# Kernel tuning notes

Measured on AMD Instinct MI355X. Metric: run time of the kernel, lower is better.

The kernel has to match this reference:

```python
import jax, jax.numpy as jnp
import numpy as np

B, N = 16, 200000
R = 1_000_000
ITERS = 5
DAMPING = 0.5


def setup_inputs() -> dict:
    key = jax.random.key(0)
    ks = jax.random.split(key, 7)
    return {
        "evidence_logits": jax.random.normal(ks[0], (B, N), dtype=jnp.float32),
        "weights_t1": jax.random.uniform(ks[1], (R,), dtype=jnp.float32),
        "weights_t2": jax.random.uniform(ks[2], (R,), dtype=jnp.float32),
        "weights_t3": jax.random.uniform(ks[3], (R,), dtype=jnp.float32),
        "indices_t1": jax.random.randint(ks[4], (R, 2), 0, N, dtype=jnp.int64) if jax.config.jax_enable_x64 else jax.random.randint(ks[4], (R, 2), 0, N, dtype=jnp.int32),
        "indices_t2": jax.random.randint(ks[5], (R, 3), 0, N, dtype=jnp.int32),
        "indices_t3": jax.random.randint(ks[6], (R, 3), 0, N, dtype=jnp.int32),
    }


def _t1_messages(q, idx, w):
    # Template T1: p_a -> p_c
    a, c = idx[:, 0], idx[:, 1]
    q_a = q[:, a]            # (B, R)
    q_c = q[:, c]
    wb = w[None, :]
    delta = jnp.zeros_like(q)
    delta = delta.at[:, c].add(wb * q_a)
    delta = delta.at[:, a].add(wb * (q_c - 1.0))
    return delta


def _t2_messages(q, idx, w):
    # Template T2: p_a ^ p_b -> p_c
    a, b, c = idx[:, 0], idx[:, 1], idx[:, 2]
    q_a, q_b, q_c = q[:, a], q[:, b], q[:, c]
    wb = w[None, :]
    delta = jnp.zeros_like(q)
    delta = delta.at[:, c].add(wb * q_a * q_b)
    delta = delta.at[:, a].add(wb * q_b * (q_c - 1.0))
    delta = delta.at[:, b].add(wb * q_a * (q_c - 1.0))
    return delta


def _t3_messages(q, idx, w):
    # Template T3: p_a ^ !p_b -> p_c
    a, b, c = idx[:, 0], idx[:, 1], idx[:, 2]
    q_a, q_b, q_c = q[:, a], q[:, b], q[:, c]
    wb = w[None, :]
    delta = jnp.zeros_like(q)
    delta = delta.at[:, c].add(wb * q_a * (1.0 - q_b))
    delta = delta.at[:, a].add(wb * (1.0 - q_b) * (q_c - 1.0))
    delta = delta.at[:, b].add(wb * q_a * (1.0 - q_c))
    return delta


def reference(evidence_logits, weights_t1, weights_t2, weights_t3,
              indices_t1, indices_t2, indices_t3):
    curr_logits = evidence_logits
    curr_q = jax.nn.sigmoid(curr_logits)
    for _ in range(ITERS):
        total = (_t1_messages(curr_q, indices_t1, weights_t1)
                 + _t2_messages(curr_q, indices_t2, weights_t2)
                 + _t3_messages(curr_q, indices_t3, weights_t3))
        target_logits = evidence_logits + total
        curr_logits = (1.0 - DAMPING) * curr_logits + DAMPING * target_logits
        curr_q = jax.nn.sigmoid(curr_logits)
    return curr_q
```

## Files before the change

### kernel.cpp

```cpp
#include <hip/hip_runtime.h>

#define B 16
#define NN 200000
#define R 1000000
#define ITERS 5
#define E_TOT (8 * R)
#define SCAN_B 1024

typedef unsigned int uint;

__device__ __forceinline__ float sigmoidf_(float x) {
    return 1.0f / (1.0f + __expf(-x));
}


__global__ void cavi_zero_u32(uint* __restrict__ p, int n) {
    int i = blockIdx.x * blockDim.x + threadIdx.x;
    if (i < n) p[i] = 0u;
}

__global__ void cavi_count(const int* __restrict__ i1, const int* __restrict__ i2,
                           const int* __restrict__ i3, uint* __restrict__ cnt) {
    int e = blockIdx.x * blockDim.x + threadIdx.x;
    if (e >= R) return;
    int a1 = i1[2 * e], c1 = i1[2 * e + 1];
    atomicAdd(&cnt[c1], 1u); atomicAdd(&cnt[a1], 1u);
    int a2 = i2[3 * e], b2 = i2[3 * e + 1], c2 = i2[3 * e + 2];
    atomicAdd(&cnt[c2], 1u); atomicAdd(&cnt[a2], 1u); atomicAdd(&cnt[b2], 1u);
    int a3 = i3[3 * e], b3 = i3[3 * e + 1], c3 = i3[3 * e + 2];
    atomicAdd(&cnt[c3], 1u); atomicAdd(&cnt[a3], 1u); atomicAdd(&cnt[b3], 1u);
}

__global__ void cavi_scan1(uint* __restrict__ cnt, uint* __restrict__ bsum) {
    __shared__ uint s[SCAN_B];
    int i = blockIdx.x * SCAN_B + threadIdx.x;
    uint v = (i < NN) ? cnt[i] : 0u;
    s[threadIdx.x] = v;
    __syncthreads();
    for (int d = 1; d < SCAN_B; d <<= 1) {
        uint t = (threadIdx.x >= d) ? s[threadIdx.x - d] : 0u;
        __syncthreads();
        s[threadIdx.x] += t;
        __syncthreads();
    }
    if (i < NN) cnt[i] = s[threadIdx.x] - v;
    if (threadIdx.x == SCAN_B - 1) bsum[blockIdx.x] = s[threadIdx.x];
}

__global__ void cavi_scan2(uint* __restrict__ bsum, int nb) {
    __shared__ uint s[256];
    uint v = (threadIdx.x < (uint)nb) ? bsum[threadIdx.x] : 0u;
    s[threadIdx.x] = v;
    __syncthreads();
    for (int d = 1; d < 256; d <<= 1) {
        uint t = (threadIdx.x >= d) ? s[threadIdx.x - d] : 0u;
        __syncthreads();
        s[threadIdx.x] += t;
        __syncthreads();
    }
    if (threadIdx.x < (uint)nb) bsum[threadIdx.x] = s[threadIdx.x] - v;
    if (threadIdx.x == 255) bsum[nb] = s[255];
}

__global__ void cavi_scan3(const uint* __restrict__ cnt, const uint* __restrict__ bsum,
                           uint* __restrict__ off, uint* __restrict__ cursor, int nb) {
    int i = blockIdx.x * blockDim.x + threadIdx.x;
    if (i < NN) {
        uint v = cnt[i] + bsum[i >> 10];
        off[i] = v;
        cursor[i] = v;
    } else if (i == NN) {
        off[NN] = bsum[nb];
    }
}

__device__ __forceinline__ void put_entry(int dest, int s1, uint md1, int s2, uint md2, float w,
                                          uint* __restrict__ cursor, uint* __restrict__ m0,
                                          uint* __restrict__ m1, float* __restrict__ wf) {
    uint pos = atomicAdd(&cursor[dest], 1u);
    m0[pos] = (uint)s1 | (md1 << 18);
    m1[pos] = (uint)s2 | (md2 << 18);
    wf[pos] = w;
}

__global__ void cavi_fill(const int* __restrict__ i1, const float* __restrict__ w1,
                          const int* __restrict__ i2, const float* __restrict__ w2,
                          const int* __restrict__ i3, const float* __restrict__ w3,
                          uint* __restrict__ cursor, uint* __restrict__ m0,
                          uint* __restrict__ m1, float* __restrict__ wf) {
    int e = blockIdx.x * blockDim.x + threadIdx.x;
    if (e >= R) return;
    {
        int a = i1[2 * e], c = i1[2 * e + 1];
        float w = w1[e];
        put_entry(c, a, 0u, 0, 3u, w, cursor, m0, m1, wf);
        put_entry(a, c, 1u, 0, 3u, w, cursor, m0, m1, wf);
    }
    {
        int a = i2[3 * e], b = i2[3 * e + 1], c = i2[3 * e + 2];
        float w = w2[e];
        put_entry(c, a, 0u, b, 0u, w, cursor, m0, m1, wf);
        put_entry(a, b, 0u, c, 1u, w, cursor, m0, m1, wf);
        put_entry(b, a, 0u, c, 1u, w, cursor, m0, m1, wf);
    }
    {
        int a = i3[3 * e], b = i3[3 * e + 1], c = i3[3 * e + 2];
        float w = w3[e];
        put_entry(c, a, 0u, b, 2u, w, cursor, m0, m1, wf);
        put_entry(a, b, 2u, c, 1u, w, cursor, m0, m1, wf);
        put_entry(b, a, 0u, c, 2u, w, cursor, m0, m1, wf);
    }
}


__global__ void cavi_init_tp(const float* __restrict__ ev, float* __restrict__ ev_nb,
                             float* __restrict__ logits_nb, float* __restrict__ q0) {
    __shared__ float lds[64 * 17];
    int n0 = blockIdx.x * 64;
    #pragma unroll
    for (int p = 0; p < 4; ++p) {
        int idx = p * 256 + threadIdx.x;
        int b = idx >> 6, i = idx & 63;
        lds[i * 17 + b] = ev[b * NN + n0 + i];
    }
    __syncthreads();
    #pragma unroll
    for (int p = 0; p < 4; ++p) {
        int j = p * 256 + threadIdx.x;
        int i = j >> 4, b = j & 15;
        float v = lds[i * 17 + b];
        int o = n0 * B + j;
        ev_nb[o] = v;
        logits_nb[o] = v;
        q0[o] = sigmoidf_(v);
    }
}

__global__ void cavi_out_tp(const float* __restrict__ q_nb, float* __restrict__ out) {
    __shared__ float lds[64 * 17];
    int n0 = blockIdx.x * 64;
    #pragma unroll
    for (int p = 0; p < 4; ++p) {
        int j = p * 256 + threadIdx.x;
        int i = j >> 4, b = j & 15;
        lds[i * 17 + b] = q_nb[n0 * B + j];
    }
    __syncthreads();
    #pragma unroll
    for (int p = 0; p < 4; ++p) {
        int idx = p * 256 + threadIdx.x;
        int b = idx >> 6, i = idx & 63;
        out[b * NN + n0 + i] = lds[i * 17 + b];
    }
}


__global__ void cavi_main(const uint* __restrict__ off,
                          const uint* __restrict__ m0, const uint* __restrict__ m1,
                          const float* __restrict__ wf,
                          const float* __restrict__ ev_nb, float* __restrict__ logits_nb,
                          const float* __restrict__ q_in, float* __restrict__ q_out) {
    int t = blockIdx.x * blockDim.x + threadIdx.x;
    if (t >= NN * B) return;
    int n = t >> 4, b = t & 15;
    uint k0 = off[n], k1 = off[n + 1];
    float acc = 0.0f;
    for (uint k = k0; k < k1; ++k) {
        uint a0 = m0[k], a1 = m1[k];
        float w = wf[k];
        float x = q_in[((a0 & 0x3FFFFu) << 4) + b];
        uint md1 = a0 >> 18;
        x = (md1 == 0u) ? x : ((md1 == 1u) ? x - 1.0f : 1.0f - x);
        uint md2 = a1 >> 18;
        float y = 1.0f;
        if (md2 != 3u) {
            float q2 = q_in[((a1 & 0x3FFFFu) << 4) + b];
            y = (md2 == 0u) ? q2 : ((md2 == 1u) ? q2 - 1.0f : 1.0f - q2);
        }
        acc = fmaf(w * x, y, acc);
    }
    float nl = 0.5f * logits_nb[t] + 0.5f * (ev_nb[t] + acc);
    logits_nb[t] = nl;
    q_out[t] = sigmoidf_(nl);
}


__global__ void fb_init(const float* __restrict__ ev, float* __restrict__ logits,
                        float* __restrict__ q_nb, float* __restrict__ delta_nb) {
    int i = blockIdx.x * blockDim.x + threadIdx.x;
    if (i >= NN * B) return;
    int b = i & 15, n = i >> 4;
    float e = ev[b * NN + n];
    logits[b * NN + n] = e;
    q_nb[i] = sigmoidf_(e);
    delta_nb[i] = 0.0f;
}

__global__ void fb_edges(const float* __restrict__ q, float* __restrict__ delta,
                         const int* __restrict__ idx1, const float* __restrict__ w1,
                         const int* __restrict__ idx2, const float* __restrict__ w2,
                         const int* __restrict__ idx3, const float* __restrict__ w3) {
    int gid = blockIdx.x * blockDim.x + threadIdx.x;
    int b = gid & 15;
    int e = gid >> 4;
    if (e >= 3 * R) return;
    if (e < R) {
        int a = idx1[e * 2 + 0], c = idx1[e * 2 + 1];
        float w = w1[e];
        float qa = q[a * B + b], qc = q[c * B + b];
        atomicAdd(&delta[c * B + b], w * qa);
        atomicAdd(&delta[a * B + b], w * (qc - 1.0f));
    } else if (e < 2 * R) {
        int ei = e - R;
        int a = idx2[ei * 3], bb = idx2[ei * 3 + 1], c = idx2[ei * 3 + 2];
        float w = w2[ei];
        float qa = q[a * B + b], qb = q[bb * B + b], qc = q[c * B + b];
        atomicAdd(&delta[c * B + b], w * qa * qb);
        atomicAdd(&delta[a * B + b], w * qb * (qc - 1.0f));
        atomicAdd(&delta[bb * B + b], w * qa * (qc - 1.0f));
    } else {
        int ei = e - 2 * R;
        int a = idx3[ei * 3], bb = idx3[ei * 3 + 1], c = idx3[ei * 3 + 2];
        float w = w3[ei];
        float qa = q[a * B + b], qb = q[bb * B + b], qc = q[c * B + b];
        atomicAdd(&delta[c * B + b], w * qa * (1.0f - qb));
        atomicAdd(&delta[a * B + b], w * (1.0f - qb) * (qc - 1.0f));
        atomicAdd(&delta[bb * B + b], w * qa * (1.0f - qc));
    }
}

__global__ void fb_update(const float* __restrict__ ev, float* __restrict__ logits,
                          float* __restrict__ q_nb, float* __restrict__ delta_nb, int write_q) {
    int i = blockIdx.x * blockDim.x + threadIdx.x;
    if (i >= NN * B) return;
    int b = i & 15, n = i >> 4;
    float d = delta_nb[i];
    delta_nb[i] = 0.0f;
    float e = ev[b * NN + n];
    float cl = logits[b * NN + n];
    float nl = 0.5f * cl + 0.5f * (e + d);
    float qv = sigmoidf_(nl);
    q_nb[i] = qv;
    logits[b * NN + n] = write_q ? qv : nl;
}


extern "C" void kernel_launch(void* const* d_in, const int* in_sizes, int n_in,
                              void* d_out, int out_size, void* d_ws, size_t ws_size,
                              hipStream_t stream) {
    const float* ev = (const float*)d_in[0];
    const float* w1 = (const float*)d_in[1];
    const float* w2 = (const float*)d_in[2];
    const float* w3 = (const float*)d_in[3];
    const int* i1 = (const int*)d_in[4];
    const int* i2 = (const int*)d_in[5];
    const int* i3 = (const int*)d_in[6];

    const size_t NB = (size_t)NN * B;

    float* ev_nb = (float*)d_ws;
    float* logits_nb = ev_nb + NB;
    float* q0 = logits_nb + NB;
    float* q1 = q0 + NB;
    uint* cnt = (uint*)(q1 + NB);
    uint* off = cnt + NN;
    uint* cursor = off + (NN + 1);
    uint* bsum = cursor + NN;
    uint* m0 = bsum + 272;
    uint* m1 = m0 + (size_t)E_TOT;
    float* wf = (float*)(m1 + (size_t)E_TOT);
    size_t needed = (size_t)((char*)(wf + (size_t)E_TOT) - (char*)d_ws);

    if (ws_size < needed) {
        float* logits = (float*)d_out;
        float* q_nb = (float*)d_ws;
        float* delta_nb = q_nb + NB;
        const int th = 256;
        const int nbg = (int)((NB + th - 1) / th);
        const int eg = (3 * R * B + th - 1) / th;
        fb_init<<<nbg, th, 0, stream>>>(ev, logits, q_nb, delta_nb);
        for (int it = 0; it < ITERS; ++it) {
            fb_edges<<<eg, th, 0, stream>>>(q_nb, delta_nb, i1, w1, i2, w2, i3, w3);
            fb_update<<<nbg, th, 0, stream>>>(ev, logits, q_nb, delta_nb, it == ITERS - 1 ? 1 : 0);
        }
        return;
    }

    const int th = 256;
    const int scan_blocks = (NN + SCAN_B - 1) / SCAN_B;

    cavi_zero_u32<<<(NN + th - 1) / th, th, 0, stream>>>(cnt, NN);
    cavi_count<<<(R + th - 1) / th, th, 0, stream>>>(i1, i2, i3, cnt);
    cavi_scan1<<<scan_blocks, SCAN_B, 0, stream>>>(cnt, bsum);
    cavi_scan2<<<1, 256, 0, stream>>>(bsum, scan_blocks);
    cavi_scan3<<<(NN + 1 + th) / th, th, 0, stream>>>(cnt, bsum, off, cursor, scan_blocks);
    cavi_fill<<<(R + th - 1) / th, th, 0, stream>>>(i1, w1, i2, w2, i3, w3, cursor, m0, m1, wf);

    cavi_init_tp<<<NN / 64, 256, 0, stream>>>(ev, ev_nb, logits_nb, q0);

    const int mg = (int)(NB / th);
    float* qi = q0;
    float* qo = q1;
    for (int it = 0; it < ITERS; ++it) {
        cavi_main<<<mg, th, 0, stream>>>(off, m0, m1, wf, ev_nb, logits_nb, qi, qo);
        float* tmp = qi; qi = qo; qo = tmp;
    }

    cavi_out_tp<<<NN / 64, 256, 0, stream>>>(qi, (float*)d_out);
}
```

Measured before the change: 2.093 ms.

## Pack CSR entries into 8 bytes and store q in half precision

Each CSR edge entry (two source indices, two mode codes, weight) is packed into one uint2, with the weight stored as fp16 instead of three separate 32-bit arrays. The q state buffers become fp16, which halves gather traffic in the main iteration kernel. The inner loop is also unrolled by two. Storing q and the weights in fp16 adds rounding error across the damped iterations, and for T1 entries the kernel now loads q[0] unconditionally and multiplies by 1.

```diff
diff --git a/kernel.cpp b/kernel.cpp
--- a/kernel.cpp
+++ b/kernel.cpp
@@ -1,4 +1,5 @@
 #include <hip/hip_runtime.h>
+#include <hip/hip_fp16.h>
 
 #define B 16
 #define NN 200000
@@ -8,6 +9,7 @@
 #define SCAN_B 1024
 
 typedef unsigned int uint;
+typedef unsigned short ushort;
 
 __device__ __forceinline__ float sigmoidf_(float x) {
     return 1.0f / (1.0f + __expf(-x));
@@ -75,46 +77,45 @@
 }
 
 __device__ __forceinline__ void put_entry(int dest, int s1, uint md1, int s2, uint md2, float w,
-                                          uint* __restrict__ cursor, uint* __restrict__ m0,
-                                          uint* __restrict__ m1, float* __restrict__ wf) {
+                                          uint* __restrict__ cursor, uint2* __restrict__ ent) {
     uint pos = atomicAdd(&cursor[dest], 1u);
-    m0[pos] = (uint)s1 | (md1 << 18);
-    m1[pos] = (uint)s2 | (md2 << 18);
-    wf[pos] = w;
+    uint lo = (uint)s1 | (md1 << 18) | (((uint)s2 & 0xFFFu) << 20);
+    uint hi = ((uint)s2 >> 12) | (md2 << 6)
+            | ((uint)__half_as_ushort(__float2half(w)) << 16);
+    ent[pos] = make_uint2(lo, hi);
 }
 
 __global__ void cavi_fill(const int* __restrict__ i1, const float* __restrict__ w1,
                           const int* __restrict__ i2, const float* __restrict__ w2,
                           const int* __restrict__ i3, const float* __restrict__ w3,
-                          uint* __restrict__ cursor, uint* __restrict__ m0,
-                          uint* __restrict__ m1, float* __restrict__ wf) {
+                          uint* __restrict__ cursor, uint2* __restrict__ ent) {
     int e = blockIdx.x * blockDim.x + threadIdx.x;
     if (e >= R) return;
     {
         int a = i1[2 * e], c = i1[2 * e + 1];
         float w = w1[e];
-        put_entry(c, a, 0u, 0, 3u, w, cursor, m0, m1, wf);
-        put_entry(a, c, 1u, 0, 3u, w, cursor, m0, m1, wf);
+        put_entry(c, a, 0u, 0, 3u, w, cursor, ent);
+        put_entry(a, c, 1u, 0, 3u, w, cursor, ent);
     }
     {
         int a = i2[3 * e], b = i2[3 * e + 1], c = i2[3 * e + 2];
         float w = w2[e];
-        put_entry(c, a, 0u, b, 0u, w, cursor, m0, m1, wf);
-        put_entry(a, b, 0u, c, 1u, w, cursor, m0, m1, wf);
-        put_entry(b, a, 0u, c, 1u, w, cursor, m0, m1, wf);
+        put_entry(c, a, 0u, b, 0u, w, cursor, ent);
+        put_entry(a, b, 0u, c, 1u, w, cursor, ent);
+        put_entry(b, a, 0u, c, 1u, w, cursor, ent);
     }
     {
         int a = i3[3 * e], b = i3[3 * e + 1], c = i3[3 * e + 2];
         float w = w3[e];
-        put_entry(c, a, 0u, b, 2u, w, cursor, m0, m1, wf);
-        put_entry(a, b, 2u, c, 1u, w, cursor, m0, m1, wf);
-        put_entry(b, a, 0u, c, 2u, w, cursor, m0, m1, wf);
+        put_entry(c, a, 0u, b, 2u, w, cursor, ent);
+        put_entry(a, b, 2u, c, 1u, w, cursor, ent);
+        put_entry(b, a, 0u, c, 2u, w, cursor, ent);
     }
 }
 
 
 __global__ void cavi_init_tp(const float* __restrict__ ev, float* __restrict__ ev_nb,
-                             float* __restrict__ logits_nb, float* __restrict__ q0) {
+                             float* __restrict__ logits_nb, __half* __restrict__ q0) {
     __shared__ float lds[64 * 17];
     int n0 = blockIdx.x * 64;
     #pragma unroll
@@ -132,18 +133,18 @@
         int o = n0 * B + j;
         ev_nb[o] = v;
         logits_nb[o] = v;
-        q0[o] = sigmoidf_(v);
-    }
-}
-
-__global__ void cavi_out_tp(const float* __restrict__ q_nb, float* __restrict__ out) {
+        q0[o] = __float2half(sigmoidf_(v));
+    }
+}
+
+__global__ void cavi_out_tp(const __half* __restrict__ q_nb, float* __restrict__ out) {
     __shared__ float lds[64 * 17];
     int n0 = blockIdx.x * 64;
     #pragma unroll
     for (int p = 0; p < 4; ++p) {
         int j = p * 256 + threadIdx.x;
         int i = j >> 4, b = j & 15;
-        lds[i * 17 + b] = q_nb[n0 * B + j];
+        lds[i * 17 + b] = __half2float(q_nb[n0 * B + j]);
     }
     __syncthreads();
     #pragma unroll
@@ -155,33 +156,43 @@
 }
 
 
-__global__ void cavi_main(const uint* __restrict__ off,
-                          const uint* __restrict__ m0, const uint* __restrict__ m1,
-                          const float* __restrict__ wf,
-                          const float* __restrict__ ev_nb, float* __restrict__ logits_nb,
-                          const float* __restrict__ q_in, float* __restrict__ q_out) {
+__device__ __forceinline__ float ent_term(uint lo, uint hi, int b,
+                                          const __half* __restrict__ q_in) {
+    int s1 = (int)(lo & 0x3FFFFu);
+    uint md1 = (lo >> 18) & 3u;
+    int s2 = (int)(((lo >> 20) & 0xFFFu) | ((hi & 0x3Fu) << 12));
+    uint md2 = (hi >> 6) & 3u;
+    float w = __half2float(__ushort_as_half((ushort)(hi >> 16)));
+    float x = __half2float(q_in[(s1 << 4) + b]);
+    x = (md1 == 0u) ? x : ((md1 == 1u) ? x - 1.0f : 1.0f - x);
+    float q2 = __half2float(q_in[(s2 << 4) + b]);
+    float y = (md2 == 0u) ? q2 : ((md2 == 1u) ? q2 - 1.0f : ((md2 == 2u) ? 1.0f - q2 : 1.0f));
+    return w * x * y;
+}
+
+__global__ __launch_bounds__(256) void cavi_main(
+        const uint* __restrict__ off, const uint2* __restrict__ ent,
+        const float* __restrict__ ev_nb, float* __restrict__ logits_nb,
+        const __half* __restrict__ q_in, __half* __restrict__ q_out) {
     int t = blockIdx.x * blockDim.x + threadIdx.x;
     if (t >= NN * B) return;
     int n = t >> 4, b = t & 15;
     uint k0 = off[n], k1 = off[n + 1];
     float acc = 0.0f;
-    for (uint k = k0; k < k1; ++k) {
-        uint a0 = m0[k], a1 = m1[k];
-        float w = wf[k];
-        float x = q_in[((a0 & 0x3FFFFu) << 4) + b];
-        uint md1 = a0 >> 18;
-        x = (md1 == 0u) ? x : ((md1 == 1u) ? x - 1.0f : 1.0f - x);
-        uint md2 = a1 >> 18;
-        float y = 1.0f;
-        if (md2 != 3u) {
-            float q2 = q_in[((a1 & 0x3FFFFu) << 4) + b];
-            y = (md2 == 0u) ? q2 : ((md2 == 1u) ? q2 - 1.0f : 1.0f - q2);
-        }
-        acc = fmaf(w * x, y, acc);
+    uint k = k0;
+    for (; k + 2 <= k1; k += 2) {
+        uint2 e0 = ent[k];
+        uint2 e1 = ent[k + 1];
+        acc += ent_term(e0.x, e0.y, b, q_in);
+        acc += ent_term(e1.x, e1.y, b, q_in);
+    }
+    if (k < k1) {
+        uint2 e0 = ent[k];
+        acc += ent_term(e0.x, e0.y, b, q_in);
     }
     float nl = 0.5f * logits_nb[t] + 0.5f * (ev_nb[t] + acc);
     logits_nb[t] = nl;
-    q_out[t] = sigmoidf_(nl);
+    q_out[t] = __float2half(sigmoidf_(nl));
 }
 
 
@@ -258,18 +269,16 @@
 
     const size_t NB = (size_t)NN * B;
 
-    float* ev_nb = (float*)d_ws;
+    uint2* ent = (uint2*)d_ws;
+    float* ev_nb = (float*)(ent + (size_t)E_TOT);
     float* logits_nb = ev_nb + NB;
-    float* q0 = logits_nb + NB;
-    float* q1 = q0 + NB;
+    __half* q0 = (__half*)(logits_nb + NB);
+    __half* q1 = q0 + NB;
     uint* cnt = (uint*)(q1 + NB);
     uint* off = cnt + NN;
     uint* cursor = off + (NN + 1);
     uint* bsum = cursor + NN;
-    uint* m0 = bsum + 272;
-    uint* m1 = m0 + (size_t)E_TOT;
-    float* wf = (float*)(m1 + (size_t)E_TOT);
-    size_t needed = (size_t)((char*)(wf + (size_t)E_TOT) - (char*)d_ws);
+    size_t needed = (size_t)((char*)(bsum + 272) - (char*)d_ws);
 
     if (ws_size < needed) {
         float* logits = (float*)d_out;
@@ -294,16 +303,16 @@
     cavi_scan1<<<scan_blocks, SCAN_B, 0, stream>>>(cnt, bsum);
     cavi_scan2<<<1, 256, 0, stream>>>(bsum, scan_blocks);
     cavi_scan3<<<(NN + 1 + th) / th, th, 0, stream>>>(cnt, bsum, off, cursor, scan_blocks);
-    cavi_fill<<<(R + th - 1) / th, th, 0, stream>>>(i1, w1, i2, w2, i3, w3, cursor, m0, m1, wf);
+    cavi_fill<<<(R + th - 1) / th, th, 0, stream>>>(i1, w1, i2, w2, i3, w3, cursor, ent);
 
     cavi_init_tp<<<NN / 64, 256, 0, stream>>>(ev, ev_nb, logits_nb, q0);
 
     const int mg = (int)(NB / th);
-    float* qi = q0;
-    float* qo = q1;
+    __half* qi = q0;
+    __half* qo = q1;
     for (int it = 0; it < ITERS; ++it) {
-        cavi_main<<<mg, th, 0, stream>>>(off, m0, m1, wf, ev_nb, logits_nb, qi, qo);
-        float* tmp = qi; qi = qo; qo = tmp;
+        cavi_main<<<mg, th, 0, stream>>>(off, ent, ev_nb, logits_nb, qi, qo);
+        __half* tmp = qi; qi = qo; qo = tmp;
     }
 
     cavi_out_tp<<<NN / 64, 256, 0, stream>>>(qi, (float*)d_out);
```

Measured after the change: 2.078 ms. No clear change (-0.7%).
